# Kernel tuning notes

Measured on AMD Instinct MI355X. Metric: run time of the kernel, lower is better.

The kernel has to match this reference:

```python
import jax, jax.numpy as jnp
import numpy as np

DIM = 128
RES = 64
H_SP, W_SP = 64, 4   # idx == 0: H_sp = resolution, W_sp = split_size
NUM_HEADS = 4
HEAD_DIM = DIM // NUM_HEADS
SCALE = HEAD_DIM ** -0.5


def img2windows(img, H_sp, W_sp):
    # img: (B, C, H, W) -> (B*nHw*nWw, H_sp*W_sp, C)
    B, C, H, W = img.shape
    x = img.reshape(B, C, H // H_sp, H_sp, W // W_sp, W_sp)
    x = jnp.transpose(x, (0, 2, 4, 3, 5, 1))
    return x.reshape(-1, H_sp * W_sp, C)


def windows2img(wins, H_sp, W_sp, H, W):
    C = wins.shape[-1]
    B = wins.shape[0] // ((H // H_sp) * (W // W_sp))
    x = wins.reshape(B, H // H_sp, W // W_sp, H_sp, W_sp, C)
    x = jnp.transpose(x, (0, 5, 1, 3, 2, 4))
    return x.reshape(B, C, H, W)


def im2cswin(x, H_sp, W_sp, num_heads):
    # (B, C, H, W) -> (B', num_heads, L, head_dim)
    C = x.shape[1]
    w = img2windows(x, H_sp, W_sp)                       # (B', L, C)
    w = w.reshape(-1, H_sp * W_sp, num_heads, C // num_heads)
    return jnp.transpose(w, (0, 2, 1, 3))


def conv1x1(x, w, b):
    # x: (B, C, H, W), w: (O, C), b: (O,)
    return jnp.einsum('bchw,oc->bohw', x, w) + b[None, :, None, None]


def depthwise5x5(x, w, b):
    # x: (B, C, H, W), w: (C, 1, 5, 5) depthwise, pad=2
    y = jax.lax.conv_general_dilated(
        x, w, window_strides=(1, 1), padding=((2, 2), (2, 2)),
        feature_group_count=x.shape[1],
        dimension_numbers=('NCHW', 'OIHW', 'NCHW'))
    return y + b[None, :, None, None]


def setup_inputs() -> dict:
    key = jax.random.key(0)
    ks = jax.random.split(key, 8)
    B = 16
    x = jax.random.normal(ks[0], (B, DIM, RES, RES), dtype=jnp.float32)
    n_windows = B * (RES // H_SP) * (RES // W_SP)
    L = H_SP * W_SP
    attn_input = jax.random.normal(ks[1], (n_windows, NUM_HEADS, L, L), dtype=jnp.float32)
    s = 0.02
    wq = jax.random.normal(ks[2], (DIM, DIM), dtype=jnp.float32) * s
    bq = jnp.zeros((DIM,), dtype=jnp.float32)
    wv = jax.random.normal(ks[3], (DIM, DIM), dtype=jnp.float32) * s
    bv = jnp.zeros((DIM,), dtype=jnp.float32)
    w_lepe = jax.random.normal(ks[4], (DIM, 1, 5, 5), dtype=jnp.float32) * s
    b_lepe = jnp.zeros((DIM,), dtype=jnp.float32)
    temperature = jnp.ones((NUM_HEADS, 1, 1), dtype=jnp.float32)
    return {"x": x, "attn_input": attn_input, "wq": wq, "bq": bq,
            "wv": wv, "bv": bv, "w_lepe": w_lepe, "b_lepe": b_lepe,
            "temperature": temperature}


def reference(x, attn_input, wq, bq, wv, bv, w_lepe, b_lepe, temperature):
    B, C, H, W = x.shape
    v_map = conv1x1(x, wv, bv)
    lepe = depthwise5x5(v_map, w_lepe, b_lepe)           # (B, C, H, W)
    # shift_size == 0: no roll
    q_map = conv1x1(x, wq, bq)
    q = im2cswin(q_map + lepe, H_SP, W_SP, NUM_HEADS) * SCALE  # (B', nh, L, d)
    k = im2cswin(x + lepe, H_SP, W_SP, NUM_HEADS)
    v = im2cswin(v_map, H_SP, W_SP, NUM_HEADS)
    scores = jnp.einsum('whqd,whkd->whqk', q, k)         # (B', nh, L, L)
    attn = jax.nn.softmax(scores, axis=-1) + temperature[None] * attn_input
    out = jnp.einsum('whqk,whkd->whqd', attn, v)         # (B', nh, L, d)
    out = jnp.transpose(out, (0, 2, 1, 3)).reshape(-1, H_SP * W_SP, C)
    out = windows2img(out, H_SP, W_SP, H, W)             # (B, C, H, W)
    return (out + lepe, attn)
```

## Files before the change

kernel.cpp:

```cpp
#include <hip/hip_runtime.h>

typedef __attribute__((ext_vector_type(4)))  float fx4;
typedef __attribute__((ext_vector_type(16))) float fx16;
typedef __attribute__((ext_vector_type(8)))  short bf8;
typedef __attribute__((ext_vector_type(4)))  short bf4;
typedef __attribute__((ext_vector_type(4)))  unsigned int u32x4;

#define SCALE 0.17677669529663687f

__device__ __forceinline__ unsigned short f2bf(float f) {
  unsigned int u = __builtin_bit_cast(unsigned int, f);
  unsigned int r = (u + 0x7fffu + ((u >> 16) & 1u)) >> 16;
  return (unsigned short)r;
}
__device__ __forceinline__ float bf2f(unsigned short u) {
  unsigned int v = ((unsigned int)u) << 16;
  return __builtin_bit_cast(float, v);
}

__global__ __launch_bounds__(256) void k0_xT(const float* __restrict__ x,
                                             unsigned short* __restrict__ xT) {
  int h = blockIdx.x, b = blockIdx.y, t = threadIdx.x;
  __shared__ unsigned short tile[128 * 68];
  const float* xrow = x + ((size_t)b * 128 * 4096) + h * 64;
#pragma unroll
  for (int i = 0; i < 8; ++i) {
    int slot = t + i * 256;
    int c = slot >> 4, wq = slot & 15;
    float4 v = *reinterpret_cast<const float4*>(xrow + (size_t)c * 4096 + wq * 4);
    unsigned short* p = &tile[c * 68 + wq * 4];
    p[0] = f2bf(v.x); p[1] = f2bf(v.y); p[2] = f2bf(v.z); p[3] = f2bf(v.w);
  }
  __syncthreads();
  int w = t >> 2, cc = t & 3;
  unsigned short tmp[32];
#pragma unroll
  for (int j = 0; j < 32; ++j) tmp[j] = tile[(cc * 32 + j) * 68 + w];
  unsigned short* dst = xT + ((size_t)(b * 4096 + h * 64 + w)) * 128 + cc * 32;
#pragma unroll
  for (int q = 0; q < 4; ++q)
    *reinterpret_cast<bf8*>(dst + q * 8) = *reinterpret_cast<bf8*>(tmp + q * 8);
}

__global__ __launch_bounds__(256) void k1_conv(const unsigned short* __restrict__ xT,
    const float* __restrict__ wq, const float* __restrict__ bq,
    const float* __restrict__ wv, const float* __restrict__ bv,
    unsigned short* __restrict__ qT, unsigned short* __restrict__ vT) {
  int pt = blockIdx.x, b = blockIdx.y, qv = blockIdx.z;
  const float* W = qv ? wv : wq;
  const float* bias = qv ? bv : bq;
  unsigned short* out = qv ? vT : qT;
  int t = threadIdx.x, lane = t & 63, wave = t >> 6;
  int wm = wave >> 1, wn = wave & 1;
  int l31 = lane & 31, g2 = lane >> 5;
  fx16 acc[2][2] = {};
  const unsigned short* Abase = xT + ((size_t)b * 4096 + pt * 128) * 128;
#pragma unroll
  for (int ks = 0; ks < 8; ++ks) {
    int kbase = ks * 16 + g2 * 8;
    bf8 a[2], bb[2];
#pragma unroll
    for (int mi = 0; mi < 2; ++mi) {
      int pix = (wm * 2 + mi) * 32 + l31;
      a[mi] = *reinterpret_cast<const bf8*>(Abase + (size_t)pix * 128 + kbase);
    }
#pragma unroll
    for (int ni = 0; ni < 2; ++ni) {
      int oc = (wn * 2 + ni) * 32 + l31;
      const float* wp = W + oc * 128 + kbase;
      float4 w0 = *reinterpret_cast<const float4*>(wp);
      float4 w1 = *reinterpret_cast<const float4*>(wp + 4);
      bf8 r;
      r[0]=(short)f2bf(w0.x); r[1]=(short)f2bf(w0.y); r[2]=(short)f2bf(w0.z); r[3]=(short)f2bf(w0.w);
      r[4]=(short)f2bf(w1.x); r[5]=(short)f2bf(w1.y); r[6]=(short)f2bf(w1.z); r[7]=(short)f2bf(w1.w);
      bb[ni] = r;
    }
#pragma unroll
    for (int mi = 0; mi < 2; ++mi)
#pragma unroll
      for (int ni = 0; ni < 2; ++ni)
        acc[mi][ni] = __builtin_amdgcn_mfma_f32_32x32x16_bf16(a[mi], bb[ni], acc[mi][ni], 0, 0, 0);
  }
#pragma unroll
  for (int ni = 0; ni < 2; ++ni) {
    int oc = (wn * 2 + ni) * 32 + l31;
    float bsv = bias[oc];
#pragma unroll
    for (int mi = 0; mi < 2; ++mi) {
#pragma unroll
      for (int r = 0; r < 16; ++r) {
        int row = (r & 3) + 8 * (r >> 2) + 4 * g2;
        int pix = pt * 128 + (wm * 2 + mi) * 32 + row;
        out[((size_t)b * 4096 + pix) * 128 + oc] = f2bf(acc[mi][ni][r] + bsv);
      }
    }
  }
}

__global__ __launch_bounds__(256) void k2_lepe(const unsigned short* __restrict__ vT,
    const float* __restrict__ wl5, const float* __restrict__ bl,
    unsigned short* __restrict__ lepe,
    unsigned short* __restrict__ kT_io, unsigned short* __restrict__ qT_io) {
  int strip = blockIdx.x, hd = blockIdx.y, b = blockIdx.z;
  int t = threadIdx.x;
  __shared__ unsigned short tile[12 * 64 * 34];
  int h0 = strip * 8;
#pragma unroll
  for (int i = 0; i < 12; ++i) {
    int slot = t + i * 256;
    int r = slot >> 8;
    int rem = slot & 255;
    int w = rem >> 2, cc = rem & 3;
    int h = h0 - 2 + r;
    unsigned short vv[8];
    if (h >= 0 && h < 64) {
      *reinterpret_cast<bf8*>(vv) = *reinterpret_cast<const bf8*>(
          vT + ((size_t)b * 4096 + h * 64 + w) * 128 + hd * 32 + cc * 8);
    } else {
#pragma unroll
      for (int j = 0; j < 8; ++j) vv[j] = 0;
    }
    unsigned int* dst = reinterpret_cast<unsigned int*>(&tile[(r * 64 + w) * 34 + cc * 8]);
#pragma unroll
    for (int j = 0; j < 4; ++j)
      dst[j] = ((unsigned int)vv[2 * j + 1] << 16) | (unsigned int)vv[2 * j];
  }
  __syncthreads();
  int c2 = t & 15, w16 = t >> 4;
  int c = c2 * 2;
  float wt0[25], wt1[25];
#pragma unroll
  for (int i = 0; i < 25; ++i) {
    wt0[i] = wl5[(hd * 32 + c) * 25 + i];
    wt1[i] = wl5[(hd * 32 + c + 1) * 25 + i];
  }
  float b0 = bl[hd * 32 + c], b1 = bl[hd * 32 + c + 1];
  for (int hh = 0; hh < 8; ++hh) {
    for (int wi = 0; wi < 4; ++wi) {
      int w = w16 * 4 + wi;
      float a0 = b0, a1 = b1;
#pragma unroll
      for (int dy = 0; dy < 5; ++dy) {
        int rr = hh + dy;
#pragma unroll
        for (int dx = 0; dx < 5; ++dx) {
          int wx = w + dx - 2;
          if (wx < 0 || wx >= 64) continue;
          unsigned int pr = *reinterpret_cast<const unsigned int*>(&tile[(rr * 64 + wx) * 34 + c]);
          float v0 = bf2f((unsigned short)(pr & 0xffffu));
          float v1 = bf2f((unsigned short)(pr >> 16));
          a0 += v0 * wt0[dy * 5 + dx];
          a1 += v1 * wt1[dy * 5 + dx];
        }
      }
      size_t po = ((size_t)b * 4096 + (h0 + hh) * 64 + w) * 128 + hd * 32 + c;
      unsigned int lp = (unsigned int)f2bf(a0) | ((unsigned int)f2bf(a1) << 16);
      *reinterpret_cast<unsigned int*>(&lepe[po]) = lp;
      unsigned int kx = *reinterpret_cast<const unsigned int*>(&kT_io[po]);
      unsigned int qx = *reinterpret_cast<const unsigned int*>(&qT_io[po]);
      unsigned int kn = (unsigned int)f2bf(bf2f((unsigned short)(kx & 0xffffu)) + a0)
                      | ((unsigned int)f2bf(bf2f((unsigned short)(kx >> 16)) + a1) << 16);
      unsigned int qn = (unsigned int)f2bf((bf2f((unsigned short)(qx & 0xffffu)) + a0) * SCALE)
                      | ((unsigned int)f2bf((bf2f((unsigned short)(qx >> 16)) + a1) * SCALE) << 16);
      *reinterpret_cast<unsigned int*>(&kT_io[po]) = kn;
      *reinterpret_cast<unsigned int*>(&qT_io[po]) = qn;
    }
  }
}

__global__ __launch_bounds__(256, 4) void k3_attn(
    const unsigned short* __restrict__ kT, const unsigned short* __restrict__ qS,
    const unsigned short* __restrict__ vT,
    const float* __restrict__ ai, const float* __restrict__ temp,
    float* __restrict__ attn, unsigned short* __restrict__ out_win) {
  int w = blockIdx.x;
  int hd = blockIdx.y;
  int b = w >> 4, ww = w & 15;
  int t = threadIdx.x, lane = t & 63, wave = t >> 6;
  int l15 = lane & 15, g = (lane >> 4) & 3;
  __shared__ unsigned short Kf[16 * 4 * 16 * 8];
  __shared__ unsigned short Vf[16 * 4 * 16 * 8];

  const size_t aBase = ((size_t)w * 4 + hd) * 65536;
  const float* aiB = ai + aBase;
  float* atB = attn + aBase;
  unsigned short* owB = out_win + ((size_t)w * 4 + hd) * 8192;

  {
    int row = t;
    int pix = (row >> 2) * 64 + ww * 4 + (row & 3);
    const unsigned short* src = kT + ((size_t)b * 4096 + pix) * 128 + hd * 32;
    int nt = row >> 4, sl = row & 15;
#pragma unroll
    for (int gg = 0; gg < 4; ++gg)
      *reinterpret_cast<bf8*>(&Kf[((nt * 4 + gg) * 16 + sl) * 8]) =
          *reinterpret_cast<const bf8*>(src + gg * 8);
  }
  {
    int row = t;
    int pix = (row >> 2) * 64 + ww * 4 + (row & 3);
    const unsigned short* src = vT + ((size_t)b * 4096 + pix) * 128 + hd * 32;
    unsigned short vv[32];
#pragma unroll
    for (int q = 0; q < 4; ++q)
      *reinterpret_cast<bf8*>(vv + q * 8) = *reinterpret_cast<const bf8*>(src + q * 8);
    int ks = row >> 5, gg = (row >> 3) & 3, j = row & 7;
#pragma unroll
    for (int d = 0; d < 32; ++d)
      Vf[(((ks * 2 + (d >> 4)) * 4 + gg) * 16 + (d & 15)) * 8 + j] = vv[d];
  }
  __syncthreads();
  float tHd = temp[hd];

  int srcA = l15 + ((lane & 16) << 1);
  int srcB = srcA + 16;
  bool ghi = (lane >= 32);

  for (int pass = 0; pass < 4; ++pass) {
    int qbase = (pass * 4 + wave) * 16;
    int qrow = qbase + l15;
    const fx4* aiRow = reinterpret_cast<const fx4*>(aiB + (size_t)qrow * 256 + g * 4);
    fx4* atRow = reinterpret_cast<fx4*>(atB + (size_t)qrow * 256 + g * 4);

    bf8 qf;
    {
      int pix = (qrow >> 2) * 64 + ww * 4 + (qrow & 3);
      qf = *reinterpret_cast<const bf8*>(
          qS + ((size_t)b * 4096 + pix) * 128 + hd * 32 + g * 8);
    }

    fx4 av[16];
#pragma unroll
    for (int nt = 0; nt < 4; ++nt) av[nt] = aiRow[nt * 4];
    asm volatile("" ::: "memory");

    fx4 acc[16];
#pragma unroll
    for (int nt = 0; nt < 16; ++nt) {
      bf8 kfr = *reinterpret_cast<const bf8*>(&Kf[((nt * 4 + g) * 16 + l15) * 8]);
      fx4 z; z[0] = 0.f; z[1] = 0.f; z[2] = 0.f; z[3] = 0.f;
      acc[nt] = __builtin_amdgcn_mfma_f32_16x16x32_bf16(kfr, qf, z, 0, 0, 0);
    }

    float m0 = fmaxf(acc[0][0], acc[0][1]), m1 = fmaxf(acc[0][2], acc[0][3]);
    float m2 = fmaxf(acc[1][0], acc[1][1]), m3 = fmaxf(acc[1][2], acc[1][3]);
#pragma unroll
    for (int nt = 2; nt < 16; nt += 2) {
      m0 = fmaxf(m0, fmaxf(acc[nt][0], acc[nt][1]));
      m1 = fmaxf(m1, fmaxf(acc[nt][2], acc[nt][3]));
      m2 = fmaxf(m2, fmaxf(acc[nt + 1][0], acc[nt + 1][1]));
      m3 = fmaxf(m3, fmaxf(acc[nt + 1][2], acc[nt + 1][3]));
    }
    float m = fmaxf(fmaxf(m0, m1), fmaxf(m2, m3));
    m = fmaxf(m, __shfl_xor(m, 16));
    m = fmaxf(m, __shfl_xor(m, 32));

    unsigned int pp0[16], pp1[16];
    float s0 = 0.f, s1 = 0.f, s2 = 0.f, s3 = 0.f;
#pragma unroll
    for (int nt = 0; nt < 16; ++nt) {
      if (nt >= 4) av[nt] = aiRow[nt * 4];
      float p0 = __expf(acc[nt][0] - m);
      float p1 = __expf(acc[nt][1] - m);
      float p2 = __expf(acc[nt][2] - m);
      float p3 = __expf(acc[nt][3] - m);
      s0 += p0; s1 += p1; s2 += p2; s3 += p3;
      pp0[nt] = (unsigned int)f2bf(p0) | ((unsigned int)f2bf(p1) << 16);
      pp1[nt] = (unsigned int)f2bf(p2) | ((unsigned int)f2bf(p3) << 16);
    }
    asm volatile("" ::: "memory");

    float s = (s0 + s1) + (s2 + s3);
    s += __shfl_xor(s, 16);
    s += __shfl_xor(s, 32);
    float inv = 1.0f / s;

#pragma unroll
    for (int nt = 0; nt < 16; ++nt) {
      fx4 a4 = av[nt];
      fx4 sv;
      sv[0] = bf2f((unsigned short)(pp0[nt] & 0xffffu)) * inv + tHd * a4[0];
      sv[1] = bf2f((unsigned short)(pp0[nt] >> 16))     * inv + tHd * a4[1];
      sv[2] = bf2f((unsigned short)(pp1[nt] & 0xffffu)) * inv + tHd * a4[2];
      sv[3] = bf2f((unsigned short)(pp1[nt] >> 16))     * inv + tHd * a4[3];
      atRow[nt * 4] = sv;
      pp0[nt] = (unsigned int)f2bf(sv[0]) | ((unsigned int)f2bf(sv[1]) << 16);
      pp1[nt] = (unsigned int)f2bf(sv[2]) | ((unsigned int)f2bf(sv[3]) << 16);
    }

    fx4 oT[2];
    oT[0][0]=0.f;oT[0][1]=0.f;oT[0][2]=0.f;oT[0][3]=0.f;
    oT[1][0]=0.f;oT[1][1]=0.f;oT[1][2]=0.f;oT[1][3]=0.f;
#pragma unroll
    for (int c = 0; c < 8; ++c) {
      int n0 = 2 * c, n1 = 2 * c + 1;
      unsigned int x0 = (unsigned int)__shfl((int)pp0[n0], srcA);
      unsigned int y0 = (unsigned int)__shfl((int)pp0[n1], srcA);
      unsigned int x1 = (unsigned int)__shfl((int)pp1[n0], srcA);
      unsigned int y1 = (unsigned int)__shfl((int)pp1[n1], srcA);
      unsigned int x2 = (unsigned int)__shfl((int)pp0[n0], srcB);
      unsigned int y2 = (unsigned int)__shfl((int)pp0[n1], srcB);
      unsigned int x3 = (unsigned int)__shfl((int)pp1[n0], srcB);
      unsigned int y3 = (unsigned int)__shfl((int)pp1[n1], srcB);
      u32x4 bw;
      bw[0] = ghi ? y0 : x0;
      bw[1] = ghi ? y1 : x1;
      bw[2] = ghi ? y2 : x2;
      bw[3] = ghi ? y3 : x3;
      bf8 pf = __builtin_bit_cast(bf8, bw);
#pragma unroll
      for (int dblk = 0; dblk < 2; ++dblk) {
        bf8 vf = *reinterpret_cast<const bf8*>(&Vf[(((c * 2 + dblk) * 4 + g) * 16 + l15) * 8]);
        oT[dblk] = __builtin_amdgcn_mfma_f32_16x16x32_bf16(vf, pf, oT[dblk], 0, 0, 0);
      }
    }
#pragma unroll
    for (int dblk = 0; dblk < 2; ++dblk) {
      unsigned int w0 = (unsigned int)f2bf(oT[dblk][0]) | ((unsigned int)f2bf(oT[dblk][1]) << 16);
      unsigned int w1 = (unsigned int)f2bf(oT[dblk][2]) | ((unsigned int)f2bf(oT[dblk][3]) << 16);
      uint2 st; st.x = w0; st.y = w1;
      *reinterpret_cast<uint2*>(&owB[(size_t)qrow * 32 + dblk * 16 + g * 4]) = st;
    }
  }
}

__global__ __launch_bounds__(256) void k4_out(const unsigned short* __restrict__ out_win,
    const unsigned short* __restrict__ lepe, float* __restrict__ out0) {
  int h = blockIdx.x, b = blockIdx.y, t = threadIdx.x;
  __shared__ float winb[16 * 533];
  __shared__ float lep[64 * 129];
#pragma unroll
  for (int i = 0; i < 4; ++i) {
    int slot = t + i * 256;
    int ww = slot >> 6, rem = slot & 63;
    int hdq = rem >> 4, rem2 = rem & 15;
    int wl = rem2 >> 2, dq = rem2 & 3;
    bf8 v = *reinterpret_cast<const bf8*>(
        out_win + (((size_t)(b * 16 + ww) * 4 + hdq) * 256 + h * 4 + wl) * 32 + dq * 8);
    float* p = &winb[ww * 533 + wl * 133 + hdq * 33 + dq * 8];
#pragma unroll
    for (int j = 0; j < 8; ++j) p[j] = bf2f((unsigned short)v[j]);
  }
#pragma unroll
  for (int i = 0; i < 4; ++i) {
    int slot = t + i * 256;
    int w = slot >> 4, cq = slot & 15;
    bf8 lv = *reinterpret_cast<const bf8*>(
        lepe + ((size_t)b * 4096 + h * 64 + w) * 128 + cq * 8);
    float* p = &lep[w * 129 + cq * 8];
#pragma unroll
    for (int j = 0; j < 8; ++j) p[j] = bf2f((unsigned short)lv[j]);
  }
  __syncthreads();
  int w = t & 63, cg = t >> 6;
#pragma unroll
  for (int ci = 0; ci < 32; ++ci) {
    int c = cg * 32 + ci;
    float val = winb[(w >> 2) * 533 + (w & 3) * 133 + (c >> 5) * 33 + (c & 31)] + lep[w * 129 + c];
    out0[((size_t)(b * 128 + c) * 64 + h) * 64 + w] = val;
  }
}

extern "C" void kernel_launch(void* const* d_in, const int* in_sizes, int n_in,
                              void* d_out, int out_size, void* d_ws, size_t ws_size,
                              hipStream_t stream) {
  const float* x    = (const float*)d_in[0];
  const float* ai   = (const float*)d_in[1];
  const float* wq   = (const float*)d_in[2];
  const float* bq   = (const float*)d_in[3];
  const float* wv   = (const float*)d_in[4];
  const float* bv   = (const float*)d_in[5];
  const float* wl5  = (const float*)d_in[6];
  const float* bl   = (const float*)d_in[7];
  const float* temp = (const float*)d_in[8];
  float* out0 = (float*)d_out;
  float* attn = out0 + 8388608;

  char* ws = (char*)d_ws;
  unsigned short* xT = (unsigned short*)(ws);
  unsigned short* qT = (unsigned short*)(ws + 16777216);
  unsigned short* vT = (unsigned short*)(ws + 33554432);
  unsigned short* lepe = (unsigned short*)(ws + 50331648);
  unsigned short* ow = (unsigned short*)(ws + 83886080);

  k0_xT  <<<dim3(64, 16),    256, 0, stream>>>(x, xT);
  k1_conv<<<dim3(32, 16, 2), 256, 0, stream>>>(xT, wq, bq, wv, bv, qT, vT);
  k2_lepe<<<dim3(8, 4, 16),  256, 0, stream>>>(vT, wl5, bl, lepe, xT, qT);
  k3_attn<<<dim3(256, 4),    256, 0, stream>>>(xT, qT, vT, ai, temp, attn, ow);
  k4_out <<<dim3(64, 16),    256, 0, stream>>>(ow, lepe, out0);
}
```

Measured before the change: 276.0 us.

## Split attention blocks into query halves, read K from global, raise occupancy

The attention kernel now launches 2048 one-dimensional blocks. Each block handles half the query rows of one window-head, in two passes instead of four, and the head index is interleaved in the block index. K fragments are loaded straight from global memory instead of staged in shared memory, which cuts LDS use. Launch bounds are raised so more blocks fit per CU. Softmax probabilities stay in fp32 registers instead of being rounded to bf16 before normalization, and the attn_input prefetch is replaced by loads inside the loop. In exchange, V staging into LDS is done twice per window-head, K reads go through cache and global memory, and the higher occupancy target may spill registers.

```diff
diff --git a/kernel.cpp b/kernel.cpp
--- a/kernel.cpp
+++ b/kernel.cpp
@@ -3,7 +3,6 @@
 typedef __attribute__((ext_vector_type(4)))  float fx4;
 typedef __attribute__((ext_vector_type(16))) float fx16;
 typedef __attribute__((ext_vector_type(8)))  short bf8;
-typedef __attribute__((ext_vector_type(4)))  short bf4;
 typedef __attribute__((ext_vector_type(4)))  unsigned int u32x4;
 
 #define SCALE 0.17677669529663687f
@@ -168,34 +167,20 @@
   }
 }
 
-__global__ __launch_bounds__(256, 4) void k3_attn(
+__global__ __launch_bounds__(256, 8) void k3_attn(
     const unsigned short* __restrict__ kT, const unsigned short* __restrict__ qS,
     const unsigned short* __restrict__ vT,
     const float* __restrict__ ai, const float* __restrict__ temp,
     float* __restrict__ attn, unsigned short* __restrict__ out_win) {
-  int w = blockIdx.x;
-  int hd = blockIdx.y;
+  int bx = blockIdx.x;
+  int half = bx >> 10;
+  int w    = (bx & 1023) >> 2;
+  int hd   = bx & 3;
   int b = w >> 4, ww = w & 15;
   int t = threadIdx.x, lane = t & 63, wave = t >> 6;
   int l15 = lane & 15, g = (lane >> 4) & 3;
-  __shared__ unsigned short Kf[16 * 4 * 16 * 8];
   __shared__ unsigned short Vf[16 * 4 * 16 * 8];
 
-  const size_t aBase = ((size_t)w * 4 + hd) * 65536;
-  const float* aiB = ai + aBase;
-  float* atB = attn + aBase;
-  unsigned short* owB = out_win + ((size_t)w * 4 + hd) * 8192;
-
-  {
-    int row = t;
-    int pix = (row >> 2) * 64 + ww * 4 + (row & 3);
-    const unsigned short* src = kT + ((size_t)b * 4096 + pix) * 128 + hd * 32;
-    int nt = row >> 4, sl = row & 15;
-#pragma unroll
-    for (int gg = 0; gg < 4; ++gg)
-      *reinterpret_cast<bf8*>(&Kf[((nt * 4 + gg) * 16 + sl) * 8]) =
-          *reinterpret_cast<const bf8*>(src + gg * 8);
-  }
   {
     int row = t;
     int pix = (row >> 2) * 64 + ww * 4 + (row & 3);
@@ -212,12 +197,20 @@
   __syncthreads();
   float tHd = temp[hd];
 
+  const size_t aBase = ((size_t)w * 4 + hd) * 65536;
+  const float* aiB = ai + aBase;
+  float* atB = attn + aBase;
+  unsigned short* owB = out_win + ((size_t)w * 4 + hd) * 8192;
+
+  const unsigned short* kfBase =
+      kT + ((size_t)b * 4096 + (l15 >> 2) * 64 + ww * 4 + (l15 & 3)) * 128 + hd * 32 + g * 8;
+
   int srcA = l15 + ((lane & 16) << 1);
   int srcB = srcA + 16;
   bool ghi = (lane >= 32);
 
-  for (int pass = 0; pass < 4; ++pass) {
-    int qbase = (pass * 4 + wave) * 16;
+  for (int sp = 0; sp < 2; ++sp) {
+    int qbase = half * 128 + sp * 64 + wave * 16;
     int qrow = qbase + l15;
     const fx4* aiRow = reinterpret_cast<const fx4*>(aiB + (size_t)qrow * 256 + g * 4);
     fx4* atRow = reinterpret_cast<fx4*>(atB + (size_t)qrow * 256 + g * 4);
@@ -229,15 +222,10 @@
           qS + ((size_t)b * 4096 + pix) * 128 + hd * 32 + g * 8);
     }
 
-    fx4 av[16];
-#pragma unroll
-    for (int nt = 0; nt < 4; ++nt) av[nt] = aiRow[nt * 4];
-    asm volatile("" ::: "memory");
-
     fx4 acc[16];
 #pragma unroll
     for (int nt = 0; nt < 16; ++nt) {
-      bf8 kfr = *reinterpret_cast<const bf8*>(&Kf[((nt * 4 + g) * 16 + l15) * 8]);
+      bf8 kfr = *reinterpret_cast<const bf8*>(kfBase + (size_t)nt * 32768);
       fx4 z; z[0] = 0.f; z[1] = 0.f; z[2] = 0.f; z[3] = 0.f;
       acc[nt] = __builtin_amdgcn_mfma_f32_16x16x32_bf16(kfr, qf, z, 0, 0, 0);
     }
@@ -255,34 +243,30 @@
     m = fmaxf(m, __shfl_xor(m, 16));
     m = fmaxf(m, __shfl_xor(m, 32));
 
-    unsigned int pp0[16], pp1[16];
     float s0 = 0.f, s1 = 0.f, s2 = 0.f, s3 = 0.f;
 #pragma unroll
     for (int nt = 0; nt < 16; ++nt) {
-      if (nt >= 4) av[nt] = aiRow[nt * 4];
       float p0 = __expf(acc[nt][0] - m);
       float p1 = __expf(acc[nt][1] - m);
       float p2 = __expf(acc[nt][2] - m);
       float p3 = __expf(acc[nt][3] - m);
+      acc[nt][0] = p0; acc[nt][1] = p1; acc[nt][2] = p2; acc[nt][3] = p3;
       s0 += p0; s1 += p1; s2 += p2; s3 += p3;
-      pp0[nt] = (unsigned int)f2bf(p0) | ((unsigned int)f2bf(p1) << 16);
-      pp1[nt] = (unsigned int)f2bf(p2) | ((unsigned int)f2bf(p3) << 16);
-    }
-    asm volatile("" ::: "memory");
-
+    }
     float s = (s0 + s1) + (s2 + s3);
     s += __shfl_xor(s, 16);
     s += __shfl_xor(s, 32);
     float inv = 1.0f / s;
 
+    unsigned int pp0[16], pp1[16];
 #pragma unroll
     for (int nt = 0; nt < 16; ++nt) {
-      fx4 a4 = av[nt];
+      fx4 a4 = aiRow[nt * 4];
       fx4 sv;
-      sv[0] = bf2f((unsigned short)(pp0[nt] & 0xffffu)) * inv + tHd * a4[0];
-      sv[1] = bf2f((unsigned short)(pp0[nt] >> 16))     * inv + tHd * a4[1];
-      sv[2] = bf2f((unsigned short)(pp1[nt] & 0xffffu)) * inv + tHd * a4[2];
-      sv[3] = bf2f((unsigned short)(pp1[nt] >> 16))     * inv + tHd * a4[3];
+      sv[0] = acc[nt][0] * inv + tHd * a4[0];
+      sv[1] = acc[nt][1] * inv + tHd * a4[1];
+      sv[2] = acc[nt][2] * inv + tHd * a4[2];
+      sv[3] = acc[nt][3] * inv + tHd * a4[3];
       atRow[nt * 4] = sv;
       pp0[nt] = (unsigned int)f2bf(sv[0]) | ((unsigned int)f2bf(sv[1]) << 16);
       pp1[nt] = (unsigned int)f2bf(sv[2]) | ((unsigned int)f2bf(sv[3]) << 16);
@@ -386,6 +370,6 @@
   k0_xT  <<<dim3(64, 16),    256, 0, stream>>>(x, xT);
   k1_conv<<<dim3(32, 16, 2), 256, 0, stream>>>(xT, wq, bq, wv, bv, qT, vT);
   k2_lepe<<<dim3(8, 4, 16),  256, 0, stream>>>(vT, wl5, bl, lepe, xT, qT);
-  k3_attn<<<dim3(256, 4),    256, 0, stream>>>(xT, qT, vT, ai, temp, attn, ow);
+  k3_attn<<<2048,            256, 0, stream>>>(xT, qT, vT, ai, temp, attn, ow);
   k4_out <<<dim3(64, 16),    256, 0, stream>>>(ow, lepe, out0);
 }
```

Measured after the change: 535.5 us. +94.0%, slower.
